# Kernel tuning notes

Measured on AMD Instinct MI355X. Metric: run time of the kernel, lower is better.

The kernel has to match this reference:

```python
import math
import jax, jax.numpy as jnp
import numpy as np

D_MODEL = 512
H = 8          # head_num
HD = 64        # head_dim
ETA = 4
R = 8
D_FFC = 2048
EPS = 1e-6
GRU_BIAS = 2.0
T, B = 128, 32
TOTAL_PROJ = H * HD * 5 + H * ETA * 3  # 2656


def _layer_norm(x, g, b):
    m = x.mean(-1, keepdims=True)
    v = ((x - m) ** 2).mean(-1, keepdims=True)
    return (x - m) / jnp.sqrt(v + 1e-5) * g + b


def _outer(a, b):
    # a: (T,B,H,D), b: (T,B,H,E) -> (T,B,H,D*E), row-major over (D,E) like torch bmm+reshape
    t, bb, h, d = a.shape
    return (a[..., :, None] * b[..., None, :]).reshape(t, bb, h, d * b.shape[-1])


def _gru_gate(x, y, w, u):
    # GTrXL-style gating: x = residual stream, y = new signal. w,u: (3, d, d)
    r = jax.nn.sigmoid(y @ w[0].T + x @ u[0].T)
    z = jax.nn.sigmoid(y @ w[1].T + x @ u[1].T - GRU_BIAS)
    h = jnp.tanh(y @ w[2].T + (r * x) @ u[2].T)
    return (1.0 - z) * x + z * h


def _discounted_sum(prev, x, d):
    # y_t = d_t * y_{t-1} + x_t, y_{-1} = prev. x: (T, ...), d broadcastable to x.
    def step(c, xd):
        xi, di = xd
        nc = di * c + xi
        return nc, nc
    _, ys = jax.lax.scan(step, prev, (x, d))
    return ys


def setup_inputs() -> dict:
    key = jax.random.key(0)
    ks = jax.random.split(key, 12)
    sc_p = 1.0 / math.sqrt(D_MODEL)
    return {
        "inputs": jax.random.normal(ks[0], (T, B, D_MODEL), jnp.float32),
        "terminations": jax.random.randint(ks[1], (T, B), 0, 2).astype(jnp.int32),
        "tilde_k": jnp.zeros((B, R, H, ETA * HD), jnp.float32),
        "tilde_v": jnp.zeros((B, R, H, HD), jnp.float32),
        "s_prev": jnp.zeros((B, H, ETA * HD), jnp.float32),
        "tick": jnp.zeros((B, 1), jnp.float32),
        "w_proj": jax.random.normal(ks[2], (TOTAL_PROJ, D_MODEL), jnp.float32) * sc_p,
        "b_proj": jnp.zeros((TOTAL_PROJ,), jnp.float32),
        "w_attn": jax.random.normal(ks[3], (D_MODEL, H * HD), jnp.float32) * (1.0 / math.sqrt(H * HD)),
        "b_attn": jnp.zeros((D_MODEL,), jnp.float32),
        "ln1_g": jnp.ones((D_MODEL,), jnp.float32),
        "ln1_b": jnp.zeros((D_MODEL,), jnp.float32),
        "ln2_g": jnp.ones((D_MODEL,), jnp.float32),
        "ln2_b": jnp.zeros((D_MODEL,), jnp.float32),
        "gru1_w": jax.random.normal(ks[4], (3, D_MODEL, D_MODEL), jnp.float32) * sc_p,
        "gru1_u": jax.random.normal(ks[5], (3, D_MODEL, D_MODEL), jnp.float32) * sc_p,
        "gru2_w": jax.random.normal(ks[6], (3, D_MODEL, D_MODEL), jnp.float32) * sc_p,
        "gru2_u": jax.random.normal(ks[7], (3, D_MODEL, D_MODEL), jnp.float32) * sc_p,
        "ffc_w1": jax.random.normal(ks[8], (D_FFC, D_MODEL), jnp.float32) * sc_p,
        "ffc_b1": jnp.zeros((D_FFC,), jnp.float32),
        "ffc_w2": jax.random.normal(ks[9], (D_MODEL, D_FFC), jnp.float32) * (1.0 / math.sqrt(D_FFC)),
        "ffc_b2": jnp.zeros((D_MODEL,), jnp.float32),
    }


def _forward(inputs, terminations, tilde_k, tilde_v, s_prev, tick,
             w_proj, b_proj, w_attn, b_attn, ln1_g, ln1_b, ln2_g, ln2_b,
             gru1_w, gru1_u, gru2_w, gru2_u, ffc_w1, ffc_b1, ffc_w2, ffc_b2):
    t, bsz, _ = inputs.shape
    omegas = jnp.linspace(-math.pi, math.pi, R).astype(inputs.dtype)

    x_normed = _layer_norm(inputs, ln1_g, ln1_b)
    all_proj = x_normed @ w_proj.T + b_proj  # (T,B,2656)
    kqv_dim = H * HD * 5
    kqvbg = all_proj[..., :kqv_dim].reshape(t, bsz, H, 5, HD)
    p123 = all_proj[..., kqv_dim:].reshape(t, bsz, H, 3, ETA)

    keys = kqvbg[..., 0, :]
    queries = kqvbg[..., 1, :]
    values = kqvbg[..., 2, :]
    beta = jax.nn.sigmoid(kqvbg[..., 3, :])
    gammas = kqvbg[..., 4, :]
    p1, p2, p3 = p123[..., 0, :], p123[..., 1, :], p123[..., 2, :]

    keys_exp = _outer(jax.nn.relu(keys), jax.nn.relu(p1))          # (T,B,H,HD*ETA)
    queries_exp = _outer(jax.nn.relu(queries), jax.nn.relu(p2))
    gammas_exp = _outer(jax.nn.sigmoid(gammas), jax.nn.sigmoid(p3))

    ticks = tick[None] + jnp.arange(1, t + 1, dtype=tick.dtype).reshape(t, 1, 1)  # (T,B,1)
    occil = jnp.cos(ticks * omegas)  # (T,B,R)

    values_gated = values * beta                 # (T,B,H,HD)
    keys_gated = keys_exp * gammas_exp           # (T,B,H,HD*ETA)
    s_in = keys_gated
    values_osc = values_gated[:, :, None] * occil[..., None, None]  # (T,B,R,H,HD)
    keys_osc = keys_gated[:, :, None] * occil[..., None, None]      # (T,B,R,H,HD*ETA)

    term_mask = (1.0 - terminations.astype(inputs.dtype))[:, :, None, None]  # (T,B,1,1)
    discount_gamma = (1.0 - gammas_exp) * term_mask   # (T,B,H,HD*ETA)
    discount_beta = (1.0 - beta) * term_mask          # (T,B,H,HD)

    final_keys = _discounted_sum(tilde_k, keys_osc, discount_gamma[:, :, None])
    final_values = _discounted_sum(tilde_v, values_osc, discount_beta[:, :, None])
    final_s = _discounted_sum(s_prev, s_in, discount_gamma)

    kdq = (final_keys * queries_exp[:, :, None]).sum(-1)   # (T,B,R,H)
    kv = (final_values * kdq[..., None]).sum(2)             # (T,B,H,HD)
    norm = (final_s * queries_exp).sum(-1) + EPS            # (T,B,H)
    attn = kv / (2 * R * norm[..., None])
    attn = attn.reshape(t, bsz, H * HD) @ w_attn.T + b_attn  # (T,B,d_model)

    gating1 = _gru_gate(inputs, jax.nn.relu(attn), gru1_w, gru1_u)
    ffc_in = _layer_norm(gating1, ln2_g, ln2_b)
    ffc_out = jax.nn.relu(jax.nn.relu(ffc_in @ ffc_w1.T + ffc_b1) @ ffc_w2.T + ffc_b2)
    output = _gru_gate(gating1, ffc_out, gru2_w, gru2_u)
    return output


def reference(inputs, terminations, tilde_k, tilde_v, s_prev, tick,
              w_proj, b_proj, w_attn, b_attn, ln1_g, ln1_b, ln2_g, ln2_b,
              gru1_w, gru1_u, gru2_w, gru2_u, ffc_w1, ffc_b1, ffc_w2, ffc_b2):
    return _forward(inputs, terminations, tilde_k, tilde_v, s_prev, tick,
                    w_proj, b_proj, w_attn, b_attn, ln1_g, ln1_b, ln2_g, ln2_b,
                    gru1_w, gru1_u, gru2_w, gru2_u, ffc_w1, ffc_b1, ffc_w2, ffc_b2)
```

## Files before the change

### kernel.cpp

```cpp
#include <hip/hip_runtime.h>
#include <hip/hip_bf16.h>
#include <math.h>

#define DM   512
#define HH   8
#define RR   8
#define TT   128
#define BBATCH 32
#define MM   (TT*BBATCH)
#define NPROJ 2656
#define KQV  2560

typedef __attribute__((ext_vector_type(8))) short bf16x8;
typedef __attribute__((ext_vector_type(4))) float f32x4;

__device__ __forceinline__ float sigmoidf_(float x) {
    return 1.0f / (1.0f + __expf(-x));
}

__device__ __forceinline__ void gload_lds16(const void* g, void* l) {
    __builtin_amdgcn_global_load_lds(
        (const __attribute__((address_space(1))) unsigned int*)g,
        (__attribute__((address_space(3))) unsigned int*)l, 16, 0, 0);
}

template<int CTRL, int RMASK>
__device__ __forceinline__ float dpp_add_(float x) {
    union { float f; int i; } a, b;
    a.f = x;
    b.i = __builtin_amdgcn_update_dpp(0, a.i, CTRL, RMASK, 0xf, true);
    return x + b.f;
}
__device__ __forceinline__ float wave_sum_u(float x) {
    x = dpp_add_<0x111, 0xf>(x);
    x = dpp_add_<0x112, 0xf>(x);
    x = dpp_add_<0x114, 0xf>(x);
    x = dpp_add_<0x118, 0xf>(x);
    x = dpp_add_<0x142, 0xa>(x);
    x = dpp_add_<0x143, 0xc>(x);
    union { float f; int i; } s, t;
    s.f = x;
    t.i = __builtin_amdgcn_readlane(s.i, 63);
    return t.f;
}

struct F2B9 {
    const float* s[9];
    __hip_bfloat16* d[9];
    int cum[10];
};

__global__ __launch_bounds__(256) void f2b_ln_all(F2B9 a,
    const float* __restrict__ x, const float* __restrict__ g,
    const float* __restrict__ b, __hip_bfloat16* __restrict__ lnout)
{
    if (blockIdx.x < 8752) {
        int q = blockIdx.x * 256 + threadIdx.x;
        if (q >= a.cum[9]) return;
        int s = 0;
        #pragma unroll
        for (int i = 1; i < 9; ++i) s += (q >= a.cum[i]);
        int i4 = (q - a.cum[s]) * 4;
        float4 v = *(const float4*)(a.s[s] + i4);
        __hip_bfloat16* dst = a.d[s] + i4;
        dst[0] = __float2bfloat16(v.x);
        dst[1] = __float2bfloat16(v.y);
        dst[2] = __float2bfloat16(v.z);
        dst[3] = __float2bfloat16(v.w);
        return;
    }
    int row = blockIdx.x - 8752;
    int tid = threadIdx.x;
    const float* xr = x + (size_t)row * DM;
    float2 v = ((const float2*)xr)[tid];
    float s = v.x + v.y;
    #pragma unroll
    for (int off = 32; off; off >>= 1) s += __shfl_down(s, off);
    __shared__ float red[8];
    int wid = tid >> 6, lane = tid & 63;
    if (lane == 0) red[wid] = s;
    __syncthreads();
    if (tid == 0) red[0] = (red[0] + red[1] + red[2] + red[3]) * (1.0f / DM);
    __syncthreads();
    float mean = red[0];
    float dx = v.x - mean, dy = v.y - mean;
    float sq = dx*dx + dy*dy;
    #pragma unroll
    for (int off = 32; off; off >>= 1) sq += __shfl_down(sq, off);
    if (lane == 0) red[4 + wid] = sq;
    __syncthreads();
    if (tid == 0) red[1] = rsqrtf((red[4]+red[5]+red[6]+red[7]) * (1.0f/DM) + 1e-5f);
    __syncthreads();
    float rstd = red[1];
    float2 gg = ((const float2*)g)[tid];
    float2 bb = ((const float2*)b)[tid];
    __hip_bfloat16* orow = lnout + (size_t)row * DM;
    orow[2*tid+0] = __float2bfloat16(dx * rstd * gg.x + bb.x);
    orow[2*tid+1] = __float2bfloat16(dy * rstd * gg.y + bb.y);
}

__global__ __launch_bounds__(256) void ln_kernel(const float* __restrict__ x,
    const float* __restrict__ g, const float* __restrict__ b,
    __hip_bfloat16* __restrict__ out)
{
    int row = blockIdx.x;
    int tid = threadIdx.x;
    const float* xr = x + (size_t)row * DM;
    float2 v = ((const float2*)xr)[tid];
    float s = v.x + v.y;
    #pragma unroll
    for (int off = 32; off; off >>= 1) s += __shfl_down(s, off);
    __shared__ float red[8];
    int wid = tid >> 6, lane = tid & 63;
    if (lane == 0) red[wid] = s;
    __syncthreads();
    if (tid == 0) red[0] = (red[0] + red[1] + red[2] + red[3]) * (1.0f / DM);
    __syncthreads();
    float mean = red[0];
    float dx = v.x - mean, dy = v.y - mean;
    float sq = dx*dx + dy*dy;
    #pragma unroll
    for (int off = 32; off; off >>= 1) sq += __shfl_down(sq, off);
    if (lane == 0) red[4 + wid] = sq;
    __syncthreads();
    if (tid == 0) red[1] = rsqrtf((red[4]+red[5]+red[6]+red[7]) * (1.0f/DM) + 1e-5f);
    __syncthreads();
    float rstd = red[1];
    float2 gg = ((const float2*)g)[tid];
    float2 bb = ((const float2*)b)[tid];
    __hip_bfloat16* orow = out + (size_t)row * DM;
    orow[2*tid+0] = __float2bfloat16(dx * rstd * gg.x + bb.x);
    orow[2*tid+1] = __float2bfloat16(dy * rstd * gg.y + bb.y);
}

__device__ __forceinline__ void gemm_core128(
    const __hip_bfloat16* __restrict__ A, const __hip_bfloat16* __restrict__ W,
    const float* __restrict__ bias,
    float* __restrict__ Cf, __hip_bfloat16* __restrict__ Cb,
    int N, int K, int act, int m0, int n0)
{
    __shared__ __attribute__((aligned(16))) __hip_bfloat16 As[8*512];
    __shared__ __attribute__((aligned(16))) __hip_bfloat16 Bs[8*512];
    int tid = threadIdx.x;
    int wave = tid >> 6, lane = tid & 63;
    int wm = (wave >> 1) * 64, wn = (wave & 1) * 64;
    int fr = lane & 15, fq = lane >> 4;

    f32x4 acc[4][4];
    #pragma unroll
    for (int i = 0; i < 4; ++i)
        #pragma unroll
        for (int j = 0; j < 4; ++j)
            acc[i][j] = (f32x4){0.f, 0.f, 0.f, 0.f};

    int sm0 = wave*16 + fr;
    int sm1 = sm0 + 64;
    int wr0 = n0 + sm0; if (wr0 >= N) wr0 = N - 1;
    int wr1 = n0 + sm1; if (wr1 >= N) wr1 = N - 1;
    const __hip_bfloat16* Ag0 = A + (size_t)(m0 + sm0) * K + fq*8;
    const __hip_bfloat16* Ag1 = A + (size_t)(m0 + sm1) * K + fq*8;
    const __hip_bfloat16* Wg0 = W + (size_t)wr0 * K + fq*8;
    const __hip_bfloat16* Wg1 = W + (size_t)wr1 * K + fq*8;

    for (int k0 = 0; k0 < K; k0 += 32) {
        gload_lds16(Ag0 + k0, As + (size_t)wave*512);
        gload_lds16(Ag1 + k0, As + (size_t)(wave+4)*512);
        gload_lds16(Wg0 + k0, Bs + (size_t)wave*512);
        gload_lds16(Wg1 + k0, Bs + (size_t)(wave+4)*512);
        __syncthreads();
        bf16x8 af[4], bfr[4];
        #pragma unroll
        for (int i = 0; i < 4; ++i) {
            af[i]  = *(const bf16x8*)(As + (size_t)(wm/16 + i)*512 + lane*8);
            bfr[i] = *(const bf16x8*)(Bs + (size_t)(wn/16 + i)*512 + lane*8);
        }
        #pragma unroll
        for (int mi = 0; mi < 4; ++mi)
            #pragma unroll
            for (int ni = 0; ni < 4; ++ni)
                acc[mi][ni] = __builtin_amdgcn_mfma_f32_16x16x32_bf16(
                    af[mi], bfr[ni], acc[mi][ni], 0, 0, 0);
        __syncthreads();
    }

    #pragma unroll
    for (int ni = 0; ni < 4; ++ni) {
        int n = n0 + wn + ni*16 + fr;
        bool nok = n < N;
        float bv = (bias && nok) ? bias[n] : 0.f;
        #pragma unroll
        for (int mi = 0; mi < 4; ++mi) {
            #pragma unroll
            for (int r = 0; r < 4; ++r) {
                int m = m0 + wm + mi*16 + fq*4 + r;
                float v = acc[mi][ni][r] + bv;
                if (act) v = fmaxf(v, 0.f);
                if (nok) {
                    size_t idx = (size_t)m * N + n;
                    if (Cf) Cf[idx] = v;
                    if (Cb) Cb[idx] = __float2bfloat16(v);
                }
            }
        }
    }
}

__global__ __launch_bounds__(256) void gemm_bf16(
    const __hip_bfloat16* __restrict__ A, const __hip_bfloat16* __restrict__ W,
    const float* __restrict__ bias,
    float* __restrict__ Cf, __hip_bfloat16* __restrict__ Cb,
    int N, int K, int act)
{
    gemm_core128(A, W, bias, Cf, Cb, N, K, act, blockIdx.y * 128, blockIdx.x * 128);
}

__global__ __launch_bounds__(256) void ffc1_bx_dual(
    const __hip_bfloat16* __restrict__ Aa, const __hip_bfloat16* __restrict__ Wa,
    const float* __restrict__ biasA, __hip_bfloat16* __restrict__ CbA,
    int Na, int splitX,
    const __hip_bfloat16* __restrict__ Ab, const __hip_bfloat16* __restrict__ Wb,
    float* __restrict__ CfB, int Nb, int K)
{
    int bx = blockIdx.x;
    if (bx < splitX)
        gemm_core128(Aa, Wa, biasA, nullptr, CbA, Na, K, 1, blockIdx.y*128, bx*128);
    else
        gemm_core128(Ab, Wb, nullptr, CfB, nullptr, Nb, K, 0, blockIdx.y*128, (bx-splitX)*128);
}

__global__ __launch_bounds__(256) void gemm_bf16_64(
    const __hip_bfloat16* __restrict__ A, const __hip_bfloat16* __restrict__ W,
    const float* __restrict__ bias,
    float* __restrict__ Cf, __hip_bfloat16* __restrict__ Cb,
    int N, int K, int act)
{
    __shared__ __attribute__((aligned(16))) __hip_bfloat16 As[4*512];
    __shared__ __attribute__((aligned(16))) __hip_bfloat16 Bs[8*512];
    int tid = threadIdx.x;
    int wave = tid >> 6, lane = tid & 63;
    int m0 = blockIdx.y * 64, n0 = blockIdx.x * 128;
    int wm = (wave >> 1) * 32, wn = (wave & 1) * 64;
    int fr = lane & 15, fq = lane >> 4;

    f32x4 acc[2][4];
    #pragma unroll
    for (int i = 0; i < 2; ++i)
        #pragma unroll
        for (int j = 0; j < 4; ++j)
            acc[i][j] = (f32x4){0.f, 0.f, 0.f, 0.f};

    const __hip_bfloat16* Ag = A + (size_t)(m0 + wave*16 + fr) * K + fq*8;
    int wr0 = n0 + wave*16 + fr; if (wr0 >= N) wr0 = N - 1;
    int wr1 = wr0 + 64;          if (wr1 >= N) wr1 = N - 1;
    const __hip_bfloat16* Wg0 = W + (size_t)wr0 * K + fq*8;
    const __hip_bfloat16* Wg1 = W + (size_t)wr1 * K + fq*8;

    for (int k0 = 0; k0 < K; k0 += 32) {
        gload_lds16(Ag  + k0, As + (size_t)wave*512);
        gload_lds16(Wg0 + k0, Bs + (size_t)wave*512);
        gload_lds16(Wg1 + k0, Bs + (size_t)(wave+4)*512);
        __syncthreads();
        bf16x8 af[2], bfr[4];
        #pragma unroll
        for (int i = 0; i < 2; ++i)
            af[i]  = *(const bf16x8*)(As + (size_t)(wm/16 + i)*512 + lane*8);
        #pragma unroll
        for (int j = 0; j < 4; ++j)
            bfr[j] = *(const bf16x8*)(Bs + (size_t)(wn/16 + j)*512 + lane*8);
        #pragma unroll
        for (int mi = 0; mi < 2; ++mi)
            #pragma unroll
            for (int ni = 0; ni < 4; ++ni)
                acc[mi][ni] = __builtin_amdgcn_mfma_f32_16x16x32_bf16(
                    af[mi], bfr[ni], acc[mi][ni], 0, 0, 0);
        __syncthreads();
    }

    #pragma unroll
    for (int ni = 0; ni < 4; ++ni) {
        int n = n0 + wn + ni*16 + fr;
        bool nok = n < N;
        float bv = (bias && nok) ? bias[n] : 0.f;
        #pragma unroll
        for (int mi = 0; mi < 2; ++mi) {
            #pragma unroll
            for (int r = 0; r < 4; ++r) {
                int m = m0 + wm + mi*16 + fq*4 + r;
                float v = acc[mi][ni][r] + bv;
                if (act) v = fmaxf(v, 0.f);
                if (nok) {
                    size_t idx = (size_t)m * N + n;
                    if (Cf) Cf[idx] = v;
                    if (Cb) Cb[idx] = __float2bfloat16(v);
                }
            }
        }
    }
}

#define NSLOT 16
#define SLOTF 912

__global__ __launch_bounds__(256) void scan_attn_fused(
    const float* __restrict__ proj, const int* __restrict__ term,
    const float* __restrict__ tick, const float* __restrict__ tilde_k,
    const float* __restrict__ tilde_v, const float* __restrict__ s_prev,
    __hip_bfloat16* __restrict__ attn,
    const __hip_bfloat16* __restrict__ gA, const __hip_bfloat16* __restrict__ gW,
    float* __restrict__ gC)
{
    int bid = blockIdx.x;
    if (bid >= 256) {
        int g = bid - 256;
        gemm_core128(gA, gW, nullptr, gC, nullptr, 1024, DM, 0,
                     (g >> 3) * 128, (g & 7) * 128);
        return;
    }

    __shared__ __attribute__((aligned(16))) float slots[NSLOT * SLOTF];
    __shared__ int prod_ctr, cons_ctr;

    const int b = bid >> 3;
    const int h = bid & 7;
    const int tid = threadIdx.x;
    const int wv = tid >> 6, lane = tid & 63;

    if (tid == 0) { prod_ctr = 0; cons_ctr = 0; }
    __syncthreads();
    if (wv >= 2) return;

    const float PI_ = 3.14159265358979323846f;

    if (wv == 1) {
        float tk = tick[b];
        int ta  = term[lane*BBATCH + b];
        int tb_ = term[(64 + lane)*BBATCH + b];
        float wv_ = -PI_ + (float)(lane & 7) * (2.0f * PI_ / 7.0f);
        float cwv = cosf(wv_), swv = sinf(wv_);
        float ocv = cosf((tk + 1.0f) * wv_), osv = sinf((tk + 1.0f) * wv_);

        for (int t0 = 0; t0 < TT; t0 += 4) {
            if (t0 >= NSLOT) {
                int tgt = t0 - (NSLOT - 4);
                while (__hip_atomic_load(&cons_ctr, __ATOMIC_ACQUIRE,
                                         __HIP_MEMORY_SCOPE_WORKGROUP) < tgt)
                    __builtin_amdgcn_s_sleep(8);
            }
            float va[4][5]; float4 P1[4], P2[4], P3[4];
            #pragma unroll
            for (int i = 0; i < 4; ++i) {
                const float* prow = proj + (size_t)((t0+i)*BBATCH + b) * NPROJ;
                const float* p5 = prow + h*320;
                va[i][0] = p5[lane];
                va[i][1] = p5[64  + lane];
                va[i][2] = p5[128 + lane];
                va[i][3] = p5[192 + lane];
                va[i][4] = p5[256 + lane];
                const float* pe = prow + KQV + h*12;
                P1[i] = *(const float4*)(pe);
                P2[i] = *(const float4*)(pe + 4);
                P3[i] = *(const float4*)(pe + 8);
            }
            #pragma unroll
            for (int i = 0; i < 4; ++i) {
                int t = t0 + i;
                int tm = (t < 64) ? __builtin_amdgcn_readlane(ta, t)
                                  : __builtin_amdgcn_readlane(tb_, t - 64);
                float mask = 1.0f - (float)tm;
                float kr = fmaxf(va[i][0], 0.f);
                float qr = fmaxf(va[i][1], 0.f);
                float sg = sigmoidf_(va[i][4]);
                float sb = sigmoidf_(va[i][3]);
                float vg = va[i][2] * sb;
                float db = (1.f - sb) * mask;
                float p1a[4] = {P1[i].x, P1[i].y, P1[i].z, P1[i].w};
                float p2a[4] = {P2[i].x, P2[i].y, P2[i].z, P2[i].w};
                float p3a[4] = {P3[i].x, P3[i].y, P3[i].z, P3[i].w};
                float4 qe, kgv, dgv;
                #pragma unroll
                for (int j = 0; j < 4; ++j) {
                    float kexp = kr * fmaxf(p1a[j], 0.f);
                    float qq   = qr * fmaxf(p2a[j], 0.f);
                    float gexp = sg * sigmoidf_(p3a[j]);
                    float kg_  = kexp * gexp;
                    float dg_  = (1.f - gexp) * mask;
                    if (j == 0) { qe.x = qq; kgv.x = kg_; dgv.x = dg_; }
                    if (j == 1) { qe.y = qq; kgv.y = kg_; dgv.y = dg_; }
                    if (j == 2) { qe.z = qq; kgv.z = kg_; dgv.z = dg_; }
                    if (j == 3) { qe.w = qq; kgv.w = kg_; dgv.w = dg_; }
                }
                float* sl = slots + (size_t)(t & (NSLOT-1)) * SLOTF;
                *(float4*)(sl + 4*lane)       = qe;
                *(float4*)(sl + 256 + 4*lane) = kgv;
                *(float4*)(sl + 512 + 4*lane) = dgv;
                sl[768 + lane] = vg;
                sl[832 + lane] = db;
                if (lane < 8) sl[896 + lane] = ocv;
                float cc = ocv, ss = osv;
                ocv = cc*cwv - ss*swv;
                osv = ss*cwv + cc*swv;
            }
            if (lane == 0)
                __hip_atomic_store(&prod_ctr, t0 + 4, __ATOMIC_RELEASE,
                                   __HIP_MEMORY_SCOPE_WORKGROUP);
        }
        return;
    }

    float4 fs = *(const float4*)(s_prev + ((size_t)(b*HH + h))*256 + lane*4);
    float4 fk[8];
    #pragma unroll
    for (int r = 0; r < 8; ++r)
        fk[r] = *(const float4*)(tilde_k + (((size_t)b*RR + r)*HH + h)*256 + lane*4);
    float fv[8];
    #pragma unroll
    for (int r = 0; r < 8; ++r)
        fv[r] = tilde_v[(((size_t)b*RR + r)*HH + h)*64 + lane];

    struct PF { float4 qe, kg, dg, o0, o1; float vg, db; };
    auto loadPF = [&](int t, PF& p) {
        if (t < TT) {
            const float* sl = slots + (size_t)(t & (NSLOT-1)) * SLOTF;
            p.qe = *(const float4*)(sl + 4*lane);
            p.kg = *(const float4*)(sl + 256 + 4*lane);
            p.dg = *(const float4*)(sl + 512 + 4*lane);
            p.vg = sl[768 + lane];
            p.db = sl[832 + lane];
            p.o0 = *(const float4*)(sl + 896);
            p.o1 = *(const float4*)(sl + 900);
        }
    };

    auto step = [&](int t, PF c) {
        float qexp[4] = {c.qe.x, c.qe.y, c.qe.z, c.qe.w};
        float kg[4]   = {c.kg.x, c.kg.y, c.kg.z, c.kg.w};
        float dg[4]   = {c.dg.x, c.dg.y, c.dg.z, c.dg.w};
        float occ[8]  = {c.o0.x, c.o0.y, c.o0.z, c.o0.w,
                         c.o1.x, c.o1.y, c.o1.z, c.o1.w};
        fs.x = dg[0]*fs.x + kg[0];
        fs.y = dg[1]*fs.y + kg[1];
        fs.z = dg[2]*fs.z + kg[2];
        fs.w = dg[3]*fs.w + kg[3];
        float snorm = fs.x*qexp[0] + fs.y*qexp[1] + fs.z*qexp[2] + fs.w*qexp[3];
        float kdq[8];
        #pragma unroll
        for (int r = 0; r < 8; ++r) {
            float4 f = fk[r];
            float o = occ[r];
            f.x = dg[0]*f.x + kg[0]*o;
            f.y = dg[1]*f.y + kg[1]*o;
            f.z = dg[2]*f.z + kg[2]*o;
            f.w = dg[3]*f.w + kg[3]*o;
            fk[r] = f;
            kdq[r] = f.x*qexp[0] + f.y*qexp[1] + f.z*qexp[2] + f.w*qexp[3];
        }
        #pragma unroll
        for (int r = 0; r < 8; ++r)
            fv[r] = c.db * fv[r] + c.vg * occ[r];
        float nrm_u = wave_sum_u(snorm);
        float kdq_u[8];
        #pragma unroll
        for (int r = 0; r < 8; ++r)
            kdq_u[r] = wave_sum_u(kdq[r]);
        float kv = 0.f;
        #pragma unroll
        for (int r = 0; r < 8; ++r)
            kv += fv[r] * kdq_u[r];
        attn[(size_t)(t*BBATCH + b)*DM + h*64 + lane] =
            __float2bfloat16(kv / (16.f * (nrm_u + 1e-6f)));
    };

    while (__hip_atomic_load(&prod_ctr, __ATOMIC_ACQUIRE,
                             __HIP_MEMORY_SCOPE_WORKGROUP) < 8)
        __builtin_amdgcn_s_sleep(2);
    PF pf0, pf1;
    loadPF(0, pf0);
    loadPF(1, pf1);

    for (int t = 0; t < TT; t += 2) {
        if ((t & 3) == 0) {
            if ((t & 7) == 0 && t >= 8 && lane == 0)
                __hip_atomic_store(&cons_ctr, t - 2, __ATOMIC_RELEASE,
                                   __HIP_MEMORY_SCOPE_WORKGROUP);
            int tgt = (t + 8 > TT) ? TT : t + 8;
            while (__hip_atomic_load(&prod_ctr, __ATOMIC_ACQUIRE,
                                     __HIP_MEMORY_SCOPE_WORKGROUP) < tgt)
                __builtin_amdgcn_s_sleep(2);
        }
        PF c0 = pf0; loadPF(t + 2, pf0);
        step(t, c0);
        PF c1 = pf1; loadPF(t + 3, pf1);
        step(t + 1, c1);
    }
}

__global__ __launch_bounds__(256) void gru_rz_kernel(const float* __restrict__ A1,
    const float* __restrict__ Bx, const float* __restrict__ x,
    __hip_bfloat16* __restrict__ rx, float* __restrict__ z)
{
    size_t i = (size_t)blockIdx.x * 256 + threadIdx.x;
    size_t m = i >> 9;
    int c = (int)(i & 511);
    float rpre = A1[m*1536 + c]       + Bx[m*1024 + c];
    float zpre = A1[m*1536 + 512 + c] + Bx[m*1024 + 512 + c] - 2.0f;
    rx[i] = __float2bfloat16(sigmoidf_(rpre) * x[i]);
    z[i]  = sigmoidf_(zpre);
}

__global__ __launch_bounds__(256) void gru_final_kernel(const float* __restrict__ A1,
    const float* __restrict__ C2, const float* __restrict__ z,
    const float* __restrict__ x, float* __restrict__ out)
{
    size_t i = (size_t)blockIdx.x * 256 + threadIdx.x;
    size_t m = i >> 9;
    int c = (int)(i & 511);
    float hh = tanhf(A1[m*1536 + 1024 + c] + C2[i]);
    float zz = z[i];
    out[i] = (1.0f - zz) * x[i] + zz * hh;
}

__global__ __launch_bounds__(256) void gru_final_ln(
    const float* __restrict__ A1, const float* __restrict__ C2,
    const float* __restrict__ z, const float* __restrict__ x,
    const float* __restrict__ g, const float* __restrict__ bta,
    float* __restrict__ g1, __hip_bfloat16* __restrict__ g1b,
    __hip_bfloat16* __restrict__ fib)
{
    int row = blockIdx.x;
    int tid = threadIdx.x;
    size_t base = (size_t)row * DM;
    float2 c2v = ((const float2*)(C2 + base))[tid];
    float2 zv  = ((const float2*)(z  + base))[tid];
    float2 xv  = ((const float2*)(x  + base))[tid];
    float2 av  = ((const float2*)(A1 + (size_t)row*1536 + 1024))[tid];
    float h0 = tanhf(av.x + c2v.x);
    float h1 = tanhf(av.y + c2v.y);
    float2 v;
    v.x = (1.0f - zv.x) * xv.x + zv.x * h0;
    v.y = (1.0f - zv.y) * xv.y + zv.y * h1;
    ((float2*)(g1 + base))[tid] = v;
    g1b[base + 2*tid+0] = __float2bfloat16(v.x);
    g1b[base + 2*tid+1] = __float2bfloat16(v.y);

    float s = v.x + v.y;
    #pragma unroll
    for (int off = 32; off; off >>= 1) s += __shfl_down(s, off);
    __shared__ float red[8];
    int wid = tid >> 6, lane = tid & 63;
    if (lane == 0) red[wid] = s;
    __syncthreads();
    if (tid == 0) red[0] = (red[0] + red[1] + red[2] + red[3]) * (1.0f / DM);
    __syncthreads();
    float mean = red[0];
    float dx = v.x - mean, dy = v.y - mean;
    float sq = dx*dx + dy*dy;
    #pragma unroll
    for (int off = 32; off; off >>= 1) sq += __shfl_down(sq, off);
    if (lane == 0) red[4 + wid] = sq;
    __syncthreads();
    if (tid == 0) red[1] = rsqrtf((red[4]+red[5]+red[6]+red[7]) * (1.0f/DM) + 1e-5f);
    __syncthreads();
    float rstd = red[1];
    float2 gg = ((const float2*)g)[tid];
    float2 bb = ((const float2*)bta)[tid];
    fib[base + 2*tid+0] = __float2bfloat16(dx * rstd * gg.x + bb.x);
    fib[base + 2*tid+1] = __float2bfloat16(dy * rstd * gg.y + bb.y);
}

extern "C" void kernel_launch(void* const* d_in, const int* in_sizes, int n_in,
                              void* d_out, int out_size, void* d_ws, size_t ws_size,
                              hipStream_t stream)
{
    const float* inputs = (const float*)d_in[0];
    const int*   term   = (const int*)  d_in[1];
    const float* tilde_k= (const float*)d_in[2];
    const float* tilde_v= (const float*)d_in[3];
    const float* s_prev = (const float*)d_in[4];
    const float* tick   = (const float*)d_in[5];
    const float* w_proj = (const float*)d_in[6];
    const float* b_proj = (const float*)d_in[7];
    const float* w_attn = (const float*)d_in[8];
    const float* b_attn = (const float*)d_in[9];
    const float* ln1_g  = (const float*)d_in[10];
    const float* ln1_b  = (const float*)d_in[11];
    const float* ln2_g  = (const float*)d_in[12];
    const float* ln2_b  = (const float*)d_in[13];
    const float* gru1_w = (const float*)d_in[14];
    const float* gru1_u = (const float*)d_in[15];
    const float* gru2_w = (const float*)d_in[16];
    const float* gru2_u = (const float*)d_in[17];
    const float* ffc_w1 = (const float*)d_in[18];
    const float* ffc_b1 = (const float*)d_in[19];
    const float* ffc_w2 = (const float*)d_in[20];
    const float* ffc_b2 = (const float*)d_in[21];
    float* out = (float*)d_out;
    float* ws  = (float*)d_ws;

    float* proj = ws;
    float* A1   = ws;
    float* C2   = ws + 10878976;
    float* zb   = ws + 12976128;
    float* g1   = ws + 15073280;
    __hip_bfloat16* bb = (__hip_bfloat16*)(ws + 17170432);
    __hip_bfloat16* wp_bf  = bb + 0;
    __hip_bfloat16* wat_bf = bb + 1359872;
    __hip_bfloat16* g1w_bf = bb + 1622016;
    __hip_bfloat16* g1u_bf = bb + 2408448;
    __hip_bfloat16* g2w_bf = bb + 3194880;
    __hip_bfloat16* g2u_bf = bb + 3981312;
    __hip_bfloat16* fw1_bf = bb + 4767744;
    __hip_bfloat16* fw2_bf = bb + 5816320;
    __hip_bfloat16* in_bf  = bb + 6864896;
    __hip_bfloat16* xn_bf  = bb + 8962048;
    __hip_bfloat16* at_bf  = bb + 11059200;
    __hip_bfloat16* y1_bf  = bb + 13156352;
    __hip_bfloat16* rx_bf  = bb + 15253504;
    __hip_bfloat16* fi_bf  = bb + 17350656;
    __hip_bfloat16* mid_bf = bb + 19447808;
    __hip_bfloat16* fo_bf  = bb + 27836416;
    __hip_bfloat16* g1_bf  = bb + 29933568;
    float* Bx = ws + 33185792;

    dim3 blk(256);

    F2B9 fa;
    const float* srcs[9] = {w_proj, w_attn, gru1_w, gru1_u, gru2_w, gru2_u,
                            ffc_w1, ffc_w2, inputs};
    __hip_bfloat16* dsts[9] = {wp_bf, wat_bf, g1w_bf, g1u_bf, g2w_bf, g2u_bf,
                               fw1_bf, fw2_bf, in_bf};
    int quads[9] = {339968, 65536, 196608, 196608, 196608, 196608,
                    262144, 262144, 524288};
    int cum = 0;
    for (int i = 0; i < 9; ++i) { fa.s[i] = srcs[i]; fa.d[i] = dsts[i]; fa.cum[i] = cum; cum += quads[i]; }
    fa.cum[9] = cum;
    f2b_ln_all<<<8752 + MM, blk, 0, stream>>>(fa, inputs, ln1_g, ln1_b, xn_bf);

    gemm_bf16<<<dim3(21, 32), blk, 0, stream>>>(xn_bf, wp_bf, b_proj, proj, nullptr, NPROJ, DM, 0);

    scan_attn_fused<<<512, blk, 0, stream>>>(proj, term, tick, tilde_k, tilde_v,
                                             s_prev, at_bf, in_bf, g1u_bf, Bx);

    gemm_bf16_64<<<dim3(4, 64), blk, 0, stream>>>(at_bf, wat_bf, b_attn, nullptr, y1_bf, DM, DM, 1);

    gemm_bf16<<<dim3(12, 32), blk, 0, stream>>>(y1_bf, g1w_bf, nullptr, A1, nullptr, 3*DM, DM, 0);
    gru_rz_kernel<<<MM*DM/256, blk, 0, stream>>>(A1, Bx, inputs, rx_bf, zb);
    gemm_bf16_64<<<dim3(4, 64), blk, 0, stream>>>(rx_bf, g1u_bf + 2*DM*DM, nullptr, C2, nullptr, DM, DM, 0);
    gru_final_ln<<<MM, blk, 0, stream>>>(A1, C2, zb, inputs, ln2_g, ln2_b, g1, g1_bf, fi_bf);

    ffc1_bx_dual<<<dim3(24, 32), blk, 0, stream>>>(fi_bf, fw1_bf, ffc_b1, mid_bf,
                                                   2048, 16,
                                                   g1_bf, g2u_bf, Bx, 1024, DM);

    gemm_bf16_64<<<dim3(4, 64), blk, 0, stream>>>(mid_bf, fw2_bf, ffc_b2, nullptr, fo_bf, DM, 2048, 1);

    gemm_bf16<<<dim3(12, 32), blk, 0, stream>>>(fo_bf, g2w_bf, nullptr, A1, nullptr, 3*DM, DM, 0);
    gru_rz_kernel<<<MM*DM/256, blk, 0, stream>>>(A1, Bx, g1, rx_bf, zb);
    gemm_bf16_64<<<dim3(4, 64), blk, 0, stream>>>(rx_bf, g2u_bf + 2*DM*DM, nullptr, C2, nullptr, DM, DM, 0);
    gru_final_kernel<<<MM*DM/256, blk, 0, stream>>>(A1, C2, zb, g1, out);
}
```

Before: 480.4 us.

## Add prefetch waves staging raw projections into LDS ahead of scan producer

Waves 2 and 3 of each scan block, which used to exit, now load the per-timestep projection rows from global memory into a small LDS ring buffer and signal readiness with per-group flags. The producer wave then reads from LDS instead of issuing global loads on its serial critical path. Shared memory moves to a dynamic allocation that the fused GEMM blocks also use, and spin-wait sleep intervals are shortened. This adds LDS use and more flag synchronisation, which could lower occupancy or add spin overhead.

```diff
diff --git a/kernel.cpp b/kernel.cpp
--- a/kernel.cpp
+++ b/kernel.cpp
@@ -99,48 +99,13 @@
     orow[2*tid+1] = __float2bfloat16(dy * rstd * gg.y + bb.y);
 }
 
-__global__ __launch_bounds__(256) void ln_kernel(const float* __restrict__ x,
-    const float* __restrict__ g, const float* __restrict__ b,
-    __hip_bfloat16* __restrict__ out)
-{
-    int row = blockIdx.x;
-    int tid = threadIdx.x;
-    const float* xr = x + (size_t)row * DM;
-    float2 v = ((const float2*)xr)[tid];
-    float s = v.x + v.y;
-    #pragma unroll
-    for (int off = 32; off; off >>= 1) s += __shfl_down(s, off);
-    __shared__ float red[8];
-    int wid = tid >> 6, lane = tid & 63;
-    if (lane == 0) red[wid] = s;
-    __syncthreads();
-    if (tid == 0) red[0] = (red[0] + red[1] + red[2] + red[3]) * (1.0f / DM);
-    __syncthreads();
-    float mean = red[0];
-    float dx = v.x - mean, dy = v.y - mean;
-    float sq = dx*dx + dy*dy;
-    #pragma unroll
-    for (int off = 32; off; off >>= 1) sq += __shfl_down(sq, off);
-    if (lane == 0) red[4 + wid] = sq;
-    __syncthreads();
-    if (tid == 0) red[1] = rsqrtf((red[4]+red[5]+red[6]+red[7]) * (1.0f/DM) + 1e-5f);
-    __syncthreads();
-    float rstd = red[1];
-    float2 gg = ((const float2*)g)[tid];
-    float2 bb = ((const float2*)b)[tid];
-    __hip_bfloat16* orow = out + (size_t)row * DM;
-    orow[2*tid+0] = __float2bfloat16(dx * rstd * gg.x + bb.x);
-    orow[2*tid+1] = __float2bfloat16(dy * rstd * gg.y + bb.y);
-}
-
 __device__ __forceinline__ void gemm_core128(
     const __hip_bfloat16* __restrict__ A, const __hip_bfloat16* __restrict__ W,
     const float* __restrict__ bias,
     float* __restrict__ Cf, __hip_bfloat16* __restrict__ Cb,
-    int N, int K, int act, int m0, int n0)
-{
-    __shared__ __attribute__((aligned(16))) __hip_bfloat16 As[8*512];
-    __shared__ __attribute__((aligned(16))) __hip_bfloat16 Bs[8*512];
+    int N, int K, int act, int m0, int n0,
+    __hip_bfloat16* As, __hip_bfloat16* Bs)
+{
     int tid = threadIdx.x;
     int wave = tid >> 6, lane = tid & 63;
     int wm = (wave >> 1) * 64, wn = (wave & 1) * 64;
@@ -211,7 +176,9 @@
     float* __restrict__ Cf, __hip_bfloat16* __restrict__ Cb,
     int N, int K, int act)
 {
-    gemm_core128(A, W, bias, Cf, Cb, N, K, act, blockIdx.y * 128, blockIdx.x * 128);
+    __shared__ __attribute__((aligned(16))) __hip_bfloat16 As[8*512];
+    __shared__ __attribute__((aligned(16))) __hip_bfloat16 Bs[8*512];
+    gemm_core128(A, W, bias, Cf, Cb, N, K, act, blockIdx.y * 128, blockIdx.x * 128, As, Bs);
 }
 
 __global__ __launch_bounds__(256) void ffc1_bx_dual(
@@ -221,11 +188,13 @@
     const __hip_bfloat16* __restrict__ Ab, const __hip_bfloat16* __restrict__ Wb,
     float* __restrict__ CfB, int Nb, int K)
 {
+    __shared__ __attribute__((aligned(16))) __hip_bfloat16 As[8*512];
+    __shared__ __attribute__((aligned(16))) __hip_bfloat16 Bs[8*512];
     int bx = blockIdx.x;
     if (bx < splitX)
-        gemm_core128(Aa, Wa, biasA, nullptr, CbA, Na, K, 1, blockIdx.y*128, bx*128);
+        gemm_core128(Aa, Wa, biasA, nullptr, CbA, Na, K, 1, blockIdx.y*128, bx*128, As, Bs);
     else
-        gemm_core128(Ab, Wb, nullptr, CfB, nullptr, Nb, K, 0, blockIdx.y*128, (bx-splitX)*128);
+        gemm_core128(Ab, Wb, nullptr, CfB, nullptr, Nb, K, 0, blockIdx.y*128, (bx-splitX)*128, As, Bs);
 }
 
 __global__ __launch_bounds__(256) void gemm_bf16_64(
@@ -300,6 +269,8 @@
 
 #define NSLOT 16
 #define SLOTF 912
+#define RSLOT 8
+#define RSLOTF 336
 
 __global__ __launch_bounds__(256) void scan_attn_fused(
     const float* __restrict__ proj, const int* __restrict__ term,
@@ -309,44 +280,44 @@
     const __hip_bfloat16* __restrict__ gA, const __hip_bfloat16* __restrict__ gW,
     float* __restrict__ gC)
 {
+    extern __shared__ __attribute__((aligned(16))) char smem_dyn[];
     int bid = blockIdx.x;
     if (bid >= 256) {
+        __hip_bfloat16* As = (__hip_bfloat16*)smem_dyn;
+        __hip_bfloat16* Bs = As + 8*512;
         int g = bid - 256;
         gemm_core128(gA, gW, nullptr, gC, nullptr, 1024, DM, 0,
-                     (g >> 3) * 128, (g & 7) * 128);
+                     (g >> 3) * 128, (g & 7) * 128, As, Bs);
         return;
     }
 
-    __shared__ __attribute__((aligned(16))) float slots[NSLOT * SLOTF];
-    __shared__ int prod_ctr, cons_ctr;
+    float* slots    = (float*)smem_dyn;
+    float* raw      = slots + NSLOT*SLOTF;
+    int*   raw_flag = (int*)(raw + RSLOT*RSLOTF);
+    int*   ctrs     = raw_flag + 32;
 
     const int b = bid >> 3;
     const int h = bid & 7;
     const int tid = threadIdx.x;
     const int wv = tid >> 6, lane = tid & 63;
 
-    if (tid == 0) { prod_ctr = 0; cons_ctr = 0; }
-    __syncthreads();
-    if (wv >= 2) return;
+    if (tid == 0) { ctrs[0] = 0; ctrs[1] = 0; }
+    if (tid < 32) raw_flag[tid] = 0;
+    __syncthreads();
+    int* prod_ctr = &ctrs[0];
+    int* cons_ctr = &ctrs[1];
 
     const float PI_ = 3.14159265358979323846f;
 
-    if (wv == 1) {
-        float tk = tick[b];
-        int ta  = term[lane*BBATCH + b];
-        int tb_ = term[(64 + lane)*BBATCH + b];
-        float wv_ = -PI_ + (float)(lane & 7) * (2.0f * PI_ / 7.0f);
-        float cwv = cosf(wv_), swv = sinf(wv_);
-        float ocv = cosf((tk + 1.0f) * wv_), osv = sinf((tk + 1.0f) * wv_);
-
-        for (int t0 = 0; t0 < TT; t0 += 4) {
-            if (t0 >= NSLOT) {
-                int tgt = t0 - (NSLOT - 4);
-                while (__hip_atomic_load(&cons_ctr, __ATOMIC_ACQUIRE,
-                                         __HIP_MEMORY_SCOPE_WORKGROUP) < tgt)
-                    __builtin_amdgcn_s_sleep(8);
-            }
-            float va[4][5]; float4 P1[4], P2[4], P3[4];
+    if (wv >= 2) {
+        for (int g = wv - 2; g < TT/4; g += 2) {
+            int t0 = g * 4;
+            if (t0 >= RSLOT) {
+                while (__hip_atomic_load(prod_ctr, __ATOMIC_ACQUIRE,
+                                         __HIP_MEMORY_SCOPE_WORKGROUP) < t0 - 4)
+                    __builtin_amdgcn_s_sleep(1);
+            }
+            float va[4][5]; float pv[4];
             #pragma unroll
             for (int i = 0; i < 4; ++i) {
                 const float* prow = proj + (size_t)((t0+i)*BBATCH + b) * NPROJ;
@@ -356,10 +327,55 @@
                 va[i][2] = p5[128 + lane];
                 va[i][3] = p5[192 + lane];
                 va[i][4] = p5[256 + lane];
-                const float* pe = prow + KQV + h*12;
-                P1[i] = *(const float4*)(pe);
-                P2[i] = *(const float4*)(pe + 4);
-                P3[i] = *(const float4*)(pe + 8);
+                pv[i] = (lane < 12) ? prow[KQV + h*12 + lane] : 0.f;
+            }
+            #pragma unroll
+            for (int i = 0; i < 4; ++i) {
+                float* rs = raw + (size_t)((t0+i) & (RSLOT-1)) * RSLOTF;
+                rs[lane]       = va[i][0];
+                rs[64  + lane] = va[i][1];
+                rs[128 + lane] = va[i][2];
+                rs[192 + lane] = va[i][3];
+                rs[256 + lane] = va[i][4];
+                if (lane < 12) rs[320 + lane] = pv[i];
+            }
+            if (lane == 0)
+                __hip_atomic_store(&raw_flag[g], 1, __ATOMIC_RELEASE,
+                                   __HIP_MEMORY_SCOPE_WORKGROUP);
+        }
+        return;
+    }
+
+    if (wv == 1) {
+        float tk = tick[b];
+        int ta  = term[lane*BBATCH + b];
+        int tb_ = term[(64 + lane)*BBATCH + b];
+        float wv_ = -PI_ + (float)(lane & 7) * (2.0f * PI_ / 7.0f);
+        float cwv = cosf(wv_), swv = sinf(wv_);
+        float ocv = cosf((tk + 1.0f) * wv_), osv = sinf((tk + 1.0f) * wv_);
+
+        for (int t0 = 0; t0 < TT; t0 += 4) {
+            if (t0 >= NSLOT) {
+                while (__hip_atomic_load(cons_ctr, __ATOMIC_ACQUIRE,
+                                         __HIP_MEMORY_SCOPE_WORKGROUP) < t0 - (NSLOT - 4))
+                    __builtin_amdgcn_s_sleep(1);
+            }
+            int g = t0 >> 2;
+            while (__hip_atomic_load(&raw_flag[g], __ATOMIC_ACQUIRE,
+                                     __HIP_MEMORY_SCOPE_WORKGROUP) == 0)
+                __builtin_amdgcn_s_sleep(1);
+            float va[4][5]; float4 P1[4], P2[4], P3[4];
+            #pragma unroll
+            for (int i = 0; i < 4; ++i) {
+                const float* rs = raw + (size_t)((t0+i) & (RSLOT-1)) * RSLOTF;
+                va[i][0] = rs[lane];
+                va[i][1] = rs[64  + lane];
+                va[i][2] = rs[128 + lane];
+                va[i][3] = rs[192 + lane];
+                va[i][4] = rs[256 + lane];
+                P1[i] = *(const float4*)(rs + 320);
+                P2[i] = *(const float4*)(rs + 324);
+                P3[i] = *(const float4*)(rs + 328);
             }
             #pragma unroll
             for (int i = 0; i < 4; ++i) {
@@ -401,7 +417,7 @@
                 osv = ss*cwv + cc*swv;
             }
             if (lane == 0)
-                __hip_atomic_store(&prod_ctr, t0 + 4, __ATOMIC_RELEASE,
+                __hip_atomic_store(prod_ctr, t0 + 4, __ATOMIC_RELEASE,
                                    __HIP_MEMORY_SCOPE_WORKGROUP);
         }
         return;
@@ -470,9 +486,9 @@
             __float2bfloat16(kv / (16.f * (nrm_u + 1e-6f)));
     };
 
-    while (__hip_atomic_load(&prod_ctr, __ATOMIC_ACQUIRE,
+    while (__hip_atomic_load(prod_ctr, __ATOMIC_ACQUIRE,
                              __HIP_MEMORY_SCOPE_WORKGROUP) < 8)
-        __builtin_amdgcn_s_sleep(2);
+        __builtin_amdgcn_s_sleep(1);
     PF pf0, pf1;
     loadPF(0, pf0);
     loadPF(1, pf1);
@@ -480,12 +496,12 @@
     for (int t = 0; t < TT; t += 2) {
         if ((t & 3) == 0) {
             if ((t & 7) == 0 && t >= 8 && lane == 0)
-                __hip_atomic_store(&cons_ctr, t - 2, __ATOMIC_RELEASE,
+                __hip_atomic_store(cons_ctr, t - 2, __ATOMIC_RELEASE,
                                    __HIP_MEMORY_SCOPE_WORKGROUP);
             int tgt = (t + 8 > TT) ? TT : t + 8;
-            while (__hip_atomic_load(&prod_ctr, __ATOMIC_ACQUIRE,
+            while (__hip_atomic_load(prod_ctr, __ATOMIC_ACQUIRE,
                                      __HIP_MEMORY_SCOPE_WORKGROUP) < tgt)
-                __builtin_amdgcn_s_sleep(2);
+                __builtin_amdgcn_s_sleep(1);
         }
         PF c0 = pf0; loadPF(t + 2, pf0);
         step(t, c0);
@@ -637,8 +653,9 @@
 
     gemm_bf16<<<dim3(21, 32), blk, 0, stream>>>(xn_bf, wp_bf, b_proj, proj, nullptr, NPROJ, DM, 0);
 
-    scan_attn_fused<<<512, blk, 0, stream>>>(proj, term, tick, tilde_k, tilde_v,
-                                             s_prev, at_bf, in_bf, g1u_bf, Bx);
+    size_t dyn = (size_t)(NSLOT*SLOTF + RSLOT*RSLOTF + 64) * 4;
+    scan_attn_fused<<<512, blk, dyn, stream>>>(proj, term, tick, tilde_k, tilde_v,
+                                               s_prev, at_bf, in_bf, g1u_bf, Bx);
 
     gemm_bf16_64<<<dim3(4, 64), blk, 0, stream>>>(at_bf, wat_bf, b_attn, nullptr, y1_bf, DM, DM, 1);
 
```

New measurement: 476.6 us. No clear change (-0.8%).
